# Optimization experiments

Hardware: AMD Instinct MI355X
Metric: run time of the kernel (lower is better)

## Reference

```python
import jax, jax.numpy as jnp
import numpy as np

N_NODES = 50000
N_EDGES = 800000
NFEAT = 128
NHID = 128
NCLASS = 2


def _glorot(key, shape):
    fan_in, fan_out = shape[0], shape[1]
    lim = np.sqrt(6.0 / (fan_in + fan_out)).astype(np.float32)
    return jax.random.uniform(key, shape, jnp.float32, -lim, lim)


def setup_inputs() -> dict:
    key = jax.random.key(0)
    ks = jax.random.split(key, 12)
    x = jax.random.normal(ks[0], (N_NODES, NFEAT), jnp.float32)
    edge_src = jax.random.randint(ks[1], (N_EDGES,), 0, N_NODES, jnp.int64)
    edge_dst = jax.random.randint(ks[2], (N_EDGES,), 0, N_NODES, jnp.int64)
    return {
        "x": x,
        "edge_src": edge_src,
        "edge_dst": edge_dst,
        "W1_self": _glorot(ks[3], (NFEAT, NHID)),
        "W1_neigh": _glorot(ks[4], (NFEAT, NHID)),
        "b1": jnp.zeros((NHID,), jnp.float32),
        "W2_self": _glorot(ks[5], (NHID, NHID)),
        "W2_neigh": _glorot(ks[6], (NHID, NHID)),
        "b2": jnp.zeros((NHID,), jnp.float32),
        "Wf": _glorot(ks[7], (NHID, NCLASS)),
        "bf": jnp.zeros((NCLASS,), jnp.float32),
    }


def _mean_neigh(h, edge_src, edge_dst):
    # gather source features per edge, segment-mean into destination nodes
    msgs = h[edge_src]                                   # [E, d]
    summed = jax.ops.segment_sum(msgs, edge_dst, num_segments=N_NODES)  # [N, d]
    deg = jax.ops.segment_sum(jnp.ones((edge_dst.shape[0],), h.dtype), edge_dst,
                              num_segments=N_NODES)      # [N]
    return summed / jnp.maximum(deg, 1.0)[:, None]


def _sage_conv(h, edge_src, edge_dst, W_self, W_neigh, b):
    h_neigh = _mean_neigh(h, edge_src, edge_dst)
    return h @ W_self + h_neigh @ W_neigh + b


def reference(x, edge_src, edge_dst, W1_self, W1_neigh, b1,
              W2_self, W2_neigh, b2, Wf, bf):
    h = jax.nn.relu(_sage_conv(x, edge_src, edge_dst, W1_self, W1_neigh, b1))
    # dropout is identity in eval mode
    h = _sage_conv(h, edge_src, edge_dst, W2_self, W2_neigh, b2)
    return h @ Wf + bf
```

## Files before the change

kernel.cpp:

```cpp
#include <hip/hip_runtime.h>
#include <cstdint>
#include <cstddef>

#define N_NODES 50000
#define N_EDGES 800000
#define CAP 64

#define BIN_SZ 512
#define NBIN 98
#define NSLOT 64

#define CHUNK_A 2048
#define N_PARTS 391

#define NB_PART N_PARTS
#define NB_PACK 128
#define NB_COMB 2
#define NB_PRE  (NB_PART + NB_PACK + NB_COMB)

#define NB_GEMM 391
#define NB_MAIN (NBIN * 5)

#define NB_AGG 13312

typedef __attribute__((ext_vector_type(8))) short bf16x8;
typedef __attribute__((ext_vector_type(4))) float f32x4;
typedef __attribute__((ext_vector_type(2))) float f32x2;
typedef __attribute__((ext_vector_type(4))) int   i32x4;

__device__ __forceinline__ unsigned short f2bf(float f) {
    unsigned u = __builtin_bit_cast(unsigned, f);
    u += 0x7fff + ((u >> 16) & 1);
    return (unsigned short)(u >> 16);
}
__device__ __forceinline__ float bflo(unsigned u) { return __builtin_bit_cast(float, u << 16); }
__device__ __forceinline__ float bfhi(unsigned u) { return __builtin_bit_cast(float, u & 0xffff0000u); }

__device__ __forceinline__ unsigned char f2fp8_sw(float f) {
    unsigned u = __builtin_bit_cast(unsigned, f);
    unsigned s = (u >> 24) & 0x80;
    unsigned a = u & 0x7fffffffu;
    if (a < 0x3c800000u) return (unsigned char)s;
    if (a > 0x43e00000u) a = 0x43e00000u;
    unsigned lsb = (a >> 20) & 1;
    a += 0x7ffffu + lsb;
    unsigned e = (a >> 23) - 120;
    unsigned m = (a >> 20) & 7;
    return (unsigned char)(s | (e << 3) | m);
}
__device__ __forceinline__ float fp82f_sw(unsigned b) {
    unsigned s = (b & 0x80u) << 24;
    unsigned e = (b >> 3) & 15, m = b & 7;
    if (e == 0) {
        float v = (float)m * 0.001953125f;
        return (b & 0x80u) ? -v : v;
    }
    return __builtin_bit_cast(float, s | ((e + 120) << 23) | (m << 20));
}
__device__ __forceinline__ unsigned short pk_fp8(float a, float b) {
#if __has_builtin(__builtin_amdgcn_cvt_pk_fp8_f32)
    return (unsigned short)__builtin_amdgcn_cvt_pk_fp8_f32(a, b, 0u, false);
#else
    return (unsigned short)(f2fp8_sw(a) | ((unsigned)f2fp8_sw(b) << 8));
#endif
}
__device__ __forceinline__ f32x2 unpk_fp8(unsigned short v) {
#if __has_builtin(__builtin_amdgcn_cvt_pk_f32_fp8)
    return __builtin_amdgcn_cvt_pk_f32_fp8((unsigned)v, false);
#else
    f32x2 r; r[0] = fp82f_sw(v & 0xffu); r[1] = fp82f_sw(v >> 8); return r;
#endif
}

__global__ __launch_bounds__(256) void k_pre(const int* __restrict__ src,
                                             const int* __restrict__ dst,
                                             const float* __restrict__ W1s,
                                             const float* __restrict__ W1n,
                                             const float* __restrict__ W2s,
                                             const float* __restrict__ W2n,
                                             const float* __restrict__ b2,
                                             const float* __restrict__ Wf,
                                             const float* __restrict__ bf,
                                             unsigned* __restrict__ seg,
                                             int* __restrict__ segcnt,
                                             unsigned short* __restrict__ wpack,
                                             float* __restrict__ wc) {
    int blk = blockIdx.x;
    int tid = threadIdx.x;

    if (blk < NB_PART) {
        __shared__ int hist[NBIN];
        for (int i = tid; i < NBIN; i += 256) hist[i] = 0;
        __syncthreads();
        int g = blk;
        int e0 = g * CHUNK_A + tid * 8;
        bool v = e0 < N_EDGES;
        i32x4 da = {0,0,0,0}, db = da, sa = da, sb = da;
        if (v) {
            da = *(const i32x4*)(dst + e0);
            db = *(const i32x4*)(dst + e0 + 4);
            sa = *(const i32x4*)(src + e0);
            sb = *(const i32x4*)(src + e0 + 4);
        }
        int d[8], s[8];
#pragma unroll
        for (int j = 0; j < 4; ++j) { d[j] = da[j]; s[j] = sa[j]; d[4 + j] = db[j]; s[4 + j] = sb[j]; }
#pragma unroll
        for (int j = 0; j < 8; ++j) {
            if (v) {
                int b = (int)((unsigned)d[j] >> 9);
                int lpos = atomicAdd(&hist[b], 1);
                if (lpos < NSLOT)
                    seg[((size_t)b * N_PARTS + g) * NSLOT + lpos] =
                        ((unsigned)d[j] << 16) | (unsigned)s[j];
            }
        }
        __syncthreads();
        for (int i = tid; i < NBIN; i += 256) {
            int h = hist[i];
            segcnt[i * N_PARTS + g] = h < NSLOT ? h : NSLOT;
        }
    } else if (blk < NB_PART + NB_PACK) {
        int idx = (blk - NB_PART) * 256 + tid;
        int j = idx & 7;
        int lane = (idx >> 3) & 63;
        int ks = (idx >> 9) & 7;
        int nt = idx >> 12;
        int krow = ks * 32 + ((lane >> 4) << 3) + j;
        int col = nt * 16 + (lane & 15);
        float v = (krow < 128) ? W1s[krow * 128 + col] : W1n[(krow - 128) * 128 + col];
        wpack[idx] = f2bf(v);
    } else {
        int role = blk - NB_PART - NB_PACK;
        int k = tid >> 1, c = tid & 1;
        const float* W = role == 0 ? W2s : W2n;
        float s = 0.f;
        for (int j = 0; j < 128; ++j) s += W[k * 128 + j] * Wf[j * 2 + c];
        wc[role * 256 + k * 2 + c] = s;
        if (role == 1 && tid < 2) {
            float sb = bf[tid];
            for (int j = 0; j < 128; ++j) sb += b2[j] * Wf[j * 2 + tid];
            wc[512 + tid] = sb;
        }
    }
}

__global__ __launch_bounds__(512) void k_main(const float* __restrict__ x,
                                              const unsigned* __restrict__ seg,
                                              const int* __restrict__ segcnt,
                                              const unsigned short* __restrict__ wpack,
                                              const float* __restrict__ b1,
                                              int* __restrict__ cnt,
                                              unsigned short* __restrict__ bucket,
                                              unsigned short* __restrict__ zb,
                                              unsigned char* __restrict__ yb8) {
    int blk = blockIdx.x;
    int tid = threadIdx.x;
    int G = blk / 5;
    int pos = blk - G * 5;

    if (pos == 0) {
        int b = G;
        __shared__ int cur[BIN_SZ];
        __shared__ int scnt[N_PARTS];
        for (int i = tid; i < BIN_SZ; i += 512) cur[i] = 0;
        for (int i = tid; i < N_PARTS; i += 512) scnt[i] = segcnt[b * N_PARTS + i];
        __syncthreads();
        int wave = tid >> 6, lane = tid & 63;
        const unsigned* segb = seg + (size_t)b * N_PARTS * NSLOT;
        for (int j = 0; j < 13; ++j) {
            unsigned v[4];
#pragma unroll
            for (int t = 0; t < 4; ++t) {
                int p = wave + 8 * (j * 4 + t);
                int n = p < N_PARTS ? scnt[p] : 0;
                v[t] = lane < n ? segb[(size_t)p * NSLOT + lane] : 0xffffffffu;
            }
#pragma unroll
            for (int t = 0; t < 4; ++t) {
                if (v[t] != 0xffffffffu) {
                    int d = (int)(v[t] >> 16);
                    int p = atomicAdd(&cur[d & (BIN_SZ - 1)], 1);
                    if (p < CAP) bucket[(size_t)d * CAP + p] = (unsigned short)(v[t] & 0xffffu);
                }
            }
        }
        __syncthreads();
        for (int i = tid; i < BIN_SZ; i += 512) {
            int node = (b << 9) + i;
            if (node < N_NODES) cnt[node] = cur[i];
        }
    } else {
        int g4 = G * 4 + (pos - 1);
        if (g4 >= NB_GEMM) return;
        int wid = tid >> 6;
        int lane = tid & 63;
        int l15 = lane & 15;
        int rowBase = g4 * 128 + wid * 16;
        int arow = rowBase + l15;
        if (arow >= N_NODES) arow = N_NODES - 1;
        int koff = (lane >> 4) << 3;

        const float* xrow = x + (size_t)arow * 128 + koff;
        bf16x8 a[4];
#pragma unroll
        for (int ks = 0; ks < 4; ++ks) {
            f32x4 f0 = *(const f32x4*)(xrow + ks * 32);
            f32x4 f1 = *(const f32x4*)(xrow + ks * 32 + 4);
            bf16x8 t;
            t[0] = (short)f2bf(f0[0]); t[1] = (short)f2bf(f0[1]);
            t[2] = (short)f2bf(f0[2]); t[3] = (short)f2bf(f0[3]);
            t[4] = (short)f2bf(f1[0]); t[5] = (short)f2bf(f1[1]);
            t[6] = (short)f2bf(f1[2]); t[7] = (short)f2bf(f1[3]);
            a[ks] = t;
        }

        f32x4 zacc[8] = {};
        f32x4 yacc[8] = {};
        const bf16x8* wp = (const bf16x8*)wpack + lane;
        __builtin_amdgcn_s_setprio(1);
#pragma unroll
        for (int nt = 0; nt < 8; ++nt) {
#pragma unroll
            for (int ks = 0; ks < 4; ++ks)
                zacc[nt] = __builtin_amdgcn_mfma_f32_16x16x32_bf16(a[ks], wp[(nt * 8 + ks) * 64], zacc[nt], 0, 0, 0);
#pragma unroll
            for (int ks = 0; ks < 4; ++ks)
                yacc[nt] = __builtin_amdgcn_mfma_f32_16x16x32_bf16(a[ks], wp[(nt * 8 + 4 + ks) * 64], yacc[nt], 0, 0, 0);
        }
        __builtin_amdgcn_s_setprio(0);

        int crow0 = rowBase + ((lane >> 4) << 2);
#pragma unroll
        for (int k = 0; k < 4; ++k) {
            int colA = k * 32 + l15;
            float biasA = b1[colA];
            float biasB = b1[colA + 16];
            int p2 = k * 16 + l15;
#pragma unroll
            for (int r = 0; r < 4; ++r) {
                int row = crow0 + r;
                if (row < N_NODES) {
                    unsigned zu = (unsigned)f2bf(zacc[2 * k][r] + biasA) |
                                  ((unsigned)f2bf(zacc[2 * k + 1][r] + biasB) << 16);
                    *(unsigned*)(zb + (size_t)row * 128 + 2 * p2) = zu;
                    *(unsigned short*)(yb8 + (size_t)row * 128 + 2 * p2) =
                        pk_fp8(yacc[2 * k][r], yacc[2 * k + 1][r]);
                }
            }
        }
    }
}

__global__ __launch_bounds__(256) void k_agg2(const unsigned char* __restrict__ yb8,
                                              const unsigned short* __restrict__ zb,
                                              const int* __restrict__ cnt,
                                              const unsigned short* __restrict__ bucket,
                                              const float* __restrict__ wc,
                                              float* __restrict__ pq) {
    int blk = blockIdx.x;
    int wavein = threadIdx.x >> 6;
    int lane = threadIdx.x & 63;
    int xcd = blk & 7;
    int i = (blk >> 3) * 4 + wavein;
    int b = xcd + ((i >> 9) << 3);
    if (b >= NBIN) return;
    int node = (b << 9) + (i & 511);
    if (node >= N_NODES) return;

    int deg = cnt[node];
    int colA = ((lane >> 4) << 5) + (lane & 15);
    int colB = colA + 16;
    unsigned zu = *(const unsigned*)(zb + (size_t)node * 128 + 2 * lane);
    float2 wsA = *(const float2*)(wc + 2 * colA);
    float2 wsB = *(const float2*)(wc + 2 * colB);
    float2 wnA = *(const float2*)(wc + 256 + 2 * colA);
    float2 wnB = *(const float2*)(wc + 256 + 2 * colB);

    int n = deg < CAP ? deg : CAP;
    const unsigned short* bk = bucket + (size_t)node * CAP;
    const unsigned char* ybl = yb8 + 2 * lane;
    float ax0 = 0.f, ay0 = 0.f, ax1 = 0.f, ay1 = 0.f;
    float ax2 = 0.f, ay2 = 0.f, ax3 = 0.f, ay3 = 0.f;
    int e = 0;
    for (; e + 16 <= n; e += 16) {
        uint4 ia = *(const uint4*)(bk + e);
        uint4 ib = *(const uint4*)(bk + e + 8);
        int s0  = ia.x & 0xffff, s1  = ia.x >> 16, s2  = ia.y & 0xffff, s3  = ia.y >> 16;
        int s4  = ia.z & 0xffff, s5  = ia.z >> 16, s6  = ia.w & 0xffff, s7  = ia.w >> 16;
        int s8  = ib.x & 0xffff, s9  = ib.x >> 16, s10 = ib.y & 0xffff, s11 = ib.y >> 16;
        int s12 = ib.z & 0xffff, s13 = ib.z >> 16, s14 = ib.w & 0xffff, s15 = ib.w >> 16;
        unsigned short t0  = *(const unsigned short*)(ybl + (size_t)s0  * 128);
        unsigned short t1  = *(const unsigned short*)(ybl + (size_t)s1  * 128);
        unsigned short t2  = *(const unsigned short*)(ybl + (size_t)s2  * 128);
        unsigned short t3  = *(const unsigned short*)(ybl + (size_t)s3  * 128);
        unsigned short t4  = *(const unsigned short*)(ybl + (size_t)s4  * 128);
        unsigned short t5  = *(const unsigned short*)(ybl + (size_t)s5  * 128);
        unsigned short t6  = *(const unsigned short*)(ybl + (size_t)s6  * 128);
        unsigned short t7  = *(const unsigned short*)(ybl + (size_t)s7  * 128);
        unsigned short t8  = *(const unsigned short*)(ybl + (size_t)s8  * 128);
        unsigned short t9  = *(const unsigned short*)(ybl + (size_t)s9  * 128);
        unsigned short t10 = *(const unsigned short*)(ybl + (size_t)s10 * 128);
        unsigned short t11 = *(const unsigned short*)(ybl + (size_t)s11 * 128);
        unsigned short t12 = *(const unsigned short*)(ybl + (size_t)s12 * 128);
        unsigned short t13 = *(const unsigned short*)(ybl + (size_t)s13 * 128);
        unsigned short t14 = *(const unsigned short*)(ybl + (size_t)s14 * 128);
        unsigned short t15 = *(const unsigned short*)(ybl + (size_t)s15 * 128);
        f32x2 v0 = unpk_fp8(t0),  v1 = unpk_fp8(t1),  v2 = unpk_fp8(t2),  v3 = unpk_fp8(t3);
        f32x2 v4 = unpk_fp8(t4),  v5 = unpk_fp8(t5),  v6 = unpk_fp8(t6),  v7 = unpk_fp8(t7);
        f32x2 v8 = unpk_fp8(t8),  v9 = unpk_fp8(t9),  v10 = unpk_fp8(t10), v11 = unpk_fp8(t11);
        f32x2 v12 = unpk_fp8(t12), v13 = unpk_fp8(t13), v14 = unpk_fp8(t14), v15 = unpk_fp8(t15);
        ax0 += v0[0];  ay0 += v0[1];  ax1 += v1[0];  ay1 += v1[1];
        ax2 += v2[0];  ay2 += v2[1];  ax3 += v3[0];  ay3 += v3[1];
        ax0 += v4[0];  ay0 += v4[1];  ax1 += v5[0];  ay1 += v5[1];
        ax2 += v6[0];  ay2 += v6[1];  ax3 += v7[0];  ay3 += v7[1];
        ax0 += v8[0];  ay0 += v8[1];  ax1 += v9[0];  ay1 += v9[1];
        ax2 += v10[0]; ay2 += v10[1]; ax3 += v11[0]; ay3 += v11[1];
        ax0 += v12[0]; ay0 += v12[1]; ax1 += v13[0]; ay1 += v13[1];
        ax2 += v14[0]; ay2 += v14[1]; ax3 += v15[0]; ay3 += v15[1];
    }
    if (e + 8 <= n) {
        uint4 ia = *(const uint4*)(bk + e);
        int s0 = ia.x & 0xffff, s1 = ia.x >> 16, s2 = ia.y & 0xffff, s3 = ia.y >> 16;
        int s4 = ia.z & 0xffff, s5 = ia.z >> 16, s6 = ia.w & 0xffff, s7 = ia.w >> 16;
        unsigned short t0 = *(const unsigned short*)(ybl + (size_t)s0 * 128);
        unsigned short t1 = *(const unsigned short*)(ybl + (size_t)s1 * 128);
        unsigned short t2 = *(const unsigned short*)(ybl + (size_t)s2 * 128);
        unsigned short t3 = *(const unsigned short*)(ybl + (size_t)s3 * 128);
        unsigned short t4 = *(const unsigned short*)(ybl + (size_t)s4 * 128);
        unsigned short t5 = *(const unsigned short*)(ybl + (size_t)s5 * 128);
        unsigned short t6 = *(const unsigned short*)(ybl + (size_t)s6 * 128);
        unsigned short t7 = *(const unsigned short*)(ybl + (size_t)s7 * 128);
        f32x2 v0 = unpk_fp8(t0), v1 = unpk_fp8(t1), v2 = unpk_fp8(t2), v3 = unpk_fp8(t3);
        f32x2 v4 = unpk_fp8(t4), v5 = unpk_fp8(t5), v6 = unpk_fp8(t6), v7 = unpk_fp8(t7);
        ax0 += v0[0]; ay0 += v0[1]; ax1 += v1[0]; ay1 += v1[1];
        ax2 += v2[0]; ay2 += v2[1]; ax3 += v3[0]; ay3 += v3[1];
        ax0 += v4[0]; ay0 += v4[1]; ax1 += v5[0]; ay1 += v5[1];
        ax2 += v6[0]; ay2 += v6[1]; ax3 += v7[0]; ay3 += v7[1];
        e += 8;
    }
    if (e + 4 <= n) {
        uint2 ia = *(const uint2*)(bk + e);
        int s0 = ia.x & 0xffff, s1 = ia.x >> 16, s2 = ia.y & 0xffff, s3 = ia.y >> 16;
        unsigned short t0 = *(const unsigned short*)(ybl + (size_t)s0 * 128);
        unsigned short t1 = *(const unsigned short*)(ybl + (size_t)s1 * 128);
        unsigned short t2 = *(const unsigned short*)(ybl + (size_t)s2 * 128);
        unsigned short t3 = *(const unsigned short*)(ybl + (size_t)s3 * 128);
        f32x2 v0 = unpk_fp8(t0), v1 = unpk_fp8(t1), v2 = unpk_fp8(t2), v3 = unpk_fp8(t3);
        ax0 += v0[0]; ay0 += v0[1]; ax1 += v1[0]; ay1 += v1[1];
        ax2 += v2[0]; ay2 += v2[1]; ax3 += v3[0]; ay3 += v3[1];
        e += 4;
    }
    for (; e < n; ++e) {
        unsigned short t = *(const unsigned short*)(ybl + (size_t)bk[e] * 128);
        f32x2 v = unpk_fp8(t);
        ax0 += v[0]; ay0 += v[1];
    }
    float inv = 1.0f / fmaxf((float)deg, 1.0f);
    float mx = ((ax0 + ax1) + (ax2 + ax3)) * inv;
    float my = ((ay0 + ay1) + (ay2 + ay3)) * inv;

    float h0 = fmaxf(bflo(zu) + mx, 0.f);
    float h1v = fmaxf(bfhi(zu) + my, 0.f);

    float p0 = h0 * wsA.x + h1v * wsB.x;
    float p1 = h0 * wsA.y + h1v * wsB.y;
    float q0 = h0 * wnA.x + h1v * wnB.x;
    float q1 = h0 * wnA.y + h1v * wnB.y;
#pragma unroll
    for (int off = 32; off >= 1; off >>= 1) {
        p0 += __shfl_xor(p0, off, 64);
        p1 += __shfl_xor(p1, off, 64);
        q0 += __shfl_xor(q0, off, 64);
        q1 += __shfl_xor(q1, off, 64);
    }
    if (lane == 0) {
        float4 o; o.x = p0; o.y = p1; o.z = q0; o.w = q1;
        ((float4*)pq)[node] = o;
    }
}

__global__ __launch_bounds__(256) void k_final(const float* __restrict__ pq,
                                               const int* __restrict__ cnt,
                                               const unsigned short* __restrict__ bucket,
                                               const float* __restrict__ wc,
                                               float* __restrict__ out) {
    int blk = blockIdx.x;
    int wavein = threadIdx.x >> 6;
    int lane = threadIdx.x & 63;
    int xcd = blk & 7;
    int i = (blk >> 3) * 4 + wavein;
    int b = xcd + ((i >> 9) << 3);
    if (b >= NBIN) return;
    int node = (b << 9) + (i & 511);
    if (node >= N_NODES) return;

    int deg = cnt[node];
    int n = deg < CAP ? deg : CAP;
    float qx = 0.f, qy = 0.f;
    if (lane < n) {
        int s = bucket[(size_t)node * CAP + lane];
        float2 q = *(const float2*)(pq + (size_t)s * 4 + 2);
        qx = q.x; qy = q.y;
    }
#pragma unroll
    for (int off = 32; off >= 1; off >>= 1) {
        qx += __shfl_xor(qx, off, 64);
        qy += __shfl_xor(qy, off, 64);
    }
    if (lane == 0) {
        float inv = 1.0f / fmaxf((float)deg, 1.0f);
        float2 p = *(const float2*)(pq + (size_t)node * 4);
        out[(size_t)node * 2 + 0] = p.x + qx * inv + wc[512];
        out[(size_t)node * 2 + 1] = p.y + qy * inv + wc[513];
    }
}

extern "C" void kernel_launch(void* const* d_in, const int* in_sizes, int n_in,
                              void* d_out, int out_size, void* d_ws, size_t ws_size,
                              hipStream_t stream) {
    const float* x   = (const float*)d_in[0];
    const int* esrc  = (const int*)d_in[1];
    const int* edst  = (const int*)d_in[2];
    const float* W1s = (const float*)d_in[3];
    const float* W1n = (const float*)d_in[4];
    const float* b1  = (const float*)d_in[5];
    const float* W2s = (const float*)d_in[6];
    const float* W2n = (const float*)d_in[7];
    const float* b2  = (const float*)d_in[8];
    const float* Wf  = (const float*)d_in[9];
    const float* bf  = (const float*)d_in[10];
    float* out = (float*)d_out;

    char* ws = (char*)d_ws;
    auto alloc = [&](size_t bytes) {
        char* p = ws;
        ws += (bytes + 255) & ~(size_t)255;
        return p;
    };
    int*            cnt    = (int*)           alloc((size_t)N_NODES * 4);
    unsigned short* bucket = (unsigned short*)alloc((size_t)N_NODES * CAP * 2);
    unsigned*       seg    = (unsigned*)      alloc((size_t)NBIN * N_PARTS * NSLOT * 4);
    int*            segcnt = (int*)           alloc((size_t)NBIN * N_PARTS * 4);
    unsigned short* zb     = (unsigned short*)alloc((size_t)N_NODES * 128 * 2);
    unsigned char*  yb8    = (unsigned char*) alloc((size_t)N_NODES * 128);
    unsigned short* wpack  = (unsigned short*)alloc(8 * 8 * 64 * 8 * 2);
    float*          pq     = (float*)         alloc((size_t)N_NODES * 4 * 4);
    float*          wc     = (float*)         alloc(1024 * 4);

    k_pre<<<NB_PRE, 256, 0, stream>>>(esrc, edst, W1s, W1n, W2s, W2n, b2, Wf, bf,
                                      seg, segcnt, wpack, wc);
    k_main<<<NB_MAIN, 512, 0, stream>>>(x, seg, segcnt, wpack, b1, cnt, bucket, zb, yb8);
    k_agg2<<<NB_AGG, 256, 0, stream>>>(yb8, zb, cnt, bucket, wc, pq);
    k_final<<<NB_AGG, 256, 0, stream>>>(pq, cnt, bucket, wc, out);
}
```

Before: 77.56 us.

## Fuse edge partitioning with layer-1 GEMM and pack weights into LDS per block

Restructures the kernel schedule so the edge partitioning and the dense layer-1 GEMM run in one front kernel, interleaved across blocks. Each GEMM block now packs W1 into bf16 in LDS itself, which removes the global wpack buffer and its dependency between kernels. The bucket build moves into its own small kernel. In exchange, every GEMM block redundantly converts 64KB of weights and the front kernel reserves 64KB of shared memory, which can reduce occupancy.

```diff
diff --git a/kernel.cpp b/kernel.cpp
--- a/kernel.cpp
+++ b/kernel.cpp
@@ -13,13 +13,10 @@
 #define CHUNK_A 2048
 #define N_PARTS 391
 
-#define NB_PART N_PARTS
-#define NB_PACK 128
-#define NB_COMB 2
-#define NB_PRE  (NB_PART + NB_PACK + NB_COMB)
-
 #define NB_GEMM 391
-#define NB_MAIN (NBIN * 5)
+#define NB_FRONT (2 * N_PARTS + 2)
+
+#define NB_BUILD NBIN
 
 #define NB_AGG 13312
 
@@ -72,131 +69,72 @@
 #endif
 }
 
-__global__ __launch_bounds__(256) void k_pre(const int* __restrict__ src,
-                                             const int* __restrict__ dst,
-                                             const float* __restrict__ W1s,
-                                             const float* __restrict__ W1n,
-                                             const float* __restrict__ W2s,
-                                             const float* __restrict__ W2n,
-                                             const float* __restrict__ b2,
-                                             const float* __restrict__ Wf,
-                                             const float* __restrict__ bf,
-                                             unsigned* __restrict__ seg,
-                                             int* __restrict__ segcnt,
-                                             unsigned short* __restrict__ wpack,
-                                             float* __restrict__ wc) {
+__global__ __launch_bounds__(512) void k_front(const float* __restrict__ x,
+                                               const int* __restrict__ src,
+                                               const int* __restrict__ dst,
+                                               const float* __restrict__ W1s,
+                                               const float* __restrict__ W1n,
+                                               const float* __restrict__ b1,
+                                               const float* __restrict__ W2s,
+                                               const float* __restrict__ W2n,
+                                               const float* __restrict__ b2,
+                                               const float* __restrict__ Wf,
+                                               const float* __restrict__ bf,
+                                               unsigned* __restrict__ seg,
+                                               int* __restrict__ segcnt,
+                                               unsigned short* __restrict__ zb,
+                                               unsigned char* __restrict__ yb8,
+                                               float* __restrict__ wc) {
+    __shared__ short wlds[32768];
     int blk = blockIdx.x;
     int tid = threadIdx.x;
 
-    if (blk < NB_PART) {
-        __shared__ int hist[NBIN];
-        for (int i = tid; i < NBIN; i += 256) hist[i] = 0;
+    if (blk < 2 * N_PARTS && (blk & 1) == 0) {
+        int g = blk >> 1;
+        int* hist = (int*)wlds;
+        for (int i = tid; i < NBIN; i += 512) hist[i] = 0;
         __syncthreads();
-        int g = blk;
-        int e0 = g * CHUNK_A + tid * 8;
+        int e0 = g * CHUNK_A + tid * 4;
         bool v = e0 < N_EDGES;
-        i32x4 da = {0,0,0,0}, db = da, sa = da, sb = da;
+        i32x4 d4 = {0,0,0,0}, s4 = d4;
         if (v) {
-            da = *(const i32x4*)(dst + e0);
-            db = *(const i32x4*)(dst + e0 + 4);
-            sa = *(const i32x4*)(src + e0);
-            sb = *(const i32x4*)(src + e0 + 4);
-        }
-        int d[8], s[8];
-#pragma unroll
-        for (int j = 0; j < 4; ++j) { d[j] = da[j]; s[j] = sa[j]; d[4 + j] = db[j]; s[4 + j] = sb[j]; }
-#pragma unroll
-        for (int j = 0; j < 8; ++j) {
+            d4 = *(const i32x4*)(dst + e0);
+            s4 = *(const i32x4*)(src + e0);
+        }
+#pragma unroll
+        for (int j = 0; j < 4; ++j) {
             if (v) {
-                int b = (int)((unsigned)d[j] >> 9);
+                int b = (int)((unsigned)d4[j] >> 9);
                 int lpos = atomicAdd(&hist[b], 1);
                 if (lpos < NSLOT)
                     seg[((size_t)b * N_PARTS + g) * NSLOT + lpos] =
-                        ((unsigned)d[j] << 16) | (unsigned)s[j];
+                        ((unsigned)d4[j] << 16) | (unsigned)s4[j];
             }
         }
         __syncthreads();
-        for (int i = tid; i < NBIN; i += 256) {
+        for (int i = tid; i < NBIN; i += 512) {
             int h = hist[i];
             segcnt[i * N_PARTS + g] = h < NSLOT ? h : NSLOT;
         }
-    } else if (blk < NB_PART + NB_PACK) {
-        int idx = (blk - NB_PART) * 256 + tid;
-        int j = idx & 7;
-        int lane = (idx >> 3) & 63;
-        int ks = (idx >> 9) & 7;
-        int nt = idx >> 12;
-        int krow = ks * 32 + ((lane >> 4) << 3) + j;
-        int col = nt * 16 + (lane & 15);
-        float v = (krow < 128) ? W1s[krow * 128 + col] : W1n[(krow - 128) * 128 + col];
-        wpack[idx] = f2bf(v);
-    } else {
-        int role = blk - NB_PART - NB_PACK;
-        int k = tid >> 1, c = tid & 1;
-        const float* W = role == 0 ? W2s : W2n;
-        float s = 0.f;
-        for (int j = 0; j < 128; ++j) s += W[k * 128 + j] * Wf[j * 2 + c];
-        wc[role * 256 + k * 2 + c] = s;
-        if (role == 1 && tid < 2) {
-            float sb = bf[tid];
-            for (int j = 0; j < 128; ++j) sb += b2[j] * Wf[j * 2 + tid];
-            wc[512 + tid] = sb;
-        }
-    }
-}
-
-__global__ __launch_bounds__(512) void k_main(const float* __restrict__ x,
-                                              const unsigned* __restrict__ seg,
-                                              const int* __restrict__ segcnt,
-                                              const unsigned short* __restrict__ wpack,
-                                              const float* __restrict__ b1,
-                                              int* __restrict__ cnt,
-                                              unsigned short* __restrict__ bucket,
-                                              unsigned short* __restrict__ zb,
-                                              unsigned char* __restrict__ yb8) {
-    int blk = blockIdx.x;
-    int tid = threadIdx.x;
-    int G = blk / 5;
-    int pos = blk - G * 5;
-
-    if (pos == 0) {
-        int b = G;
-        __shared__ int cur[BIN_SZ];
-        __shared__ int scnt[N_PARTS];
-        for (int i = tid; i < BIN_SZ; i += 512) cur[i] = 0;
-        for (int i = tid; i < N_PARTS; i += 512) scnt[i] = segcnt[b * N_PARTS + i];
+    } else if (blk < 2 * N_PARTS) {
+        int g4 = blk >> 1;
+        for (int i = 0; i < 64; ++i) {
+            int idx = i * 512 + tid;
+            int j = idx & 7;
+            int ln = (idx >> 3) & 63;
+            int ks = (idx >> 9) & 7;
+            int nt = idx >> 12;
+            int krow = ks * 32 + ((ln >> 4) << 3) + j;
+            int col = nt * 16 + (ln & 15);
+            float v = (krow < 128) ? W1s[krow * 128 + col] : W1n[(krow - 128) * 128 + col];
+            wlds[idx] = (short)f2bf(v);
+        }
         __syncthreads();
-        int wave = tid >> 6, lane = tid & 63;
-        const unsigned* segb = seg + (size_t)b * N_PARTS * NSLOT;
-        for (int j = 0; j < 13; ++j) {
-            unsigned v[4];
-#pragma unroll
-            for (int t = 0; t < 4; ++t) {
-                int p = wave + 8 * (j * 4 + t);
-                int n = p < N_PARTS ? scnt[p] : 0;
-                v[t] = lane < n ? segb[(size_t)p * NSLOT + lane] : 0xffffffffu;
-            }
-#pragma unroll
-            for (int t = 0; t < 4; ++t) {
-                if (v[t] != 0xffffffffu) {
-                    int d = (int)(v[t] >> 16);
-                    int p = atomicAdd(&cur[d & (BIN_SZ - 1)], 1);
-                    if (p < CAP) bucket[(size_t)d * CAP + p] = (unsigned short)(v[t] & 0xffffu);
-                }
-            }
-        }
-        __syncthreads();
-        for (int i = tid; i < BIN_SZ; i += 512) {
-            int node = (b << 9) + i;
-            if (node < N_NODES) cnt[node] = cur[i];
-        }
-    } else {
-        int g4 = G * 4 + (pos - 1);
-        if (g4 >= NB_GEMM) return;
-        int wid = tid >> 6;
+
+        int wavein = tid >> 6;
         int lane = tid & 63;
         int l15 = lane & 15;
-        int rowBase = g4 * 128 + wid * 16;
+        int rowBase = g4 * 128 + wavein * 16;
         int arow = rowBase + l15;
         if (arow >= N_NODES) arow = N_NODES - 1;
         int koff = (lane >> 4) << 3;
@@ -217,7 +155,7 @@
 
         f32x4 zacc[8] = {};
         f32x4 yacc[8] = {};
-        const bf16x8* wp = (const bf16x8*)wpack + lane;
+        const bf16x8* wp = (const bf16x8*)wlds + lane;
         __builtin_amdgcn_s_setprio(1);
 #pragma unroll
         for (int nt = 0; nt < 8; ++nt) {
@@ -249,6 +187,57 @@
                 }
             }
         }
+    } else {
+        int role = blk - 2 * N_PARTS;
+        if (tid < 256) {
+            int k = tid >> 1, c = tid & 1;
+            const float* W = role == 0 ? W2s : W2n;
+            float s = 0.f;
+            for (int j = 0; j < 128; ++j) s += W[k * 128 + j] * Wf[j * 2 + c];
+            wc[role * 256 + k * 2 + c] = s;
+            if (role == 1 && tid < 2) {
+                float sb = bf[tid];
+                for (int j = 0; j < 128; ++j) sb += b2[j] * Wf[j * 2 + tid];
+                wc[512 + tid] = sb;
+            }
+        }
+    }
+}
+
+__global__ __launch_bounds__(512) void k_build(const unsigned* __restrict__ seg,
+                                               const int* __restrict__ segcnt,
+                                               int* __restrict__ cnt,
+                                               unsigned short* __restrict__ bucket) {
+    int b = blockIdx.x;
+    int tid = threadIdx.x;
+    __shared__ int cur[BIN_SZ];
+    __shared__ int scnt[N_PARTS];
+    for (int i = tid; i < BIN_SZ; i += 512) cur[i] = 0;
+    for (int i = tid; i < N_PARTS; i += 512) scnt[i] = segcnt[b * N_PARTS + i];
+    __syncthreads();
+    int wave = tid >> 6, lane = tid & 63;
+    const unsigned* segb = seg + (size_t)b * N_PARTS * NSLOT;
+    for (int j = 0; j < 13; ++j) {
+        unsigned v[4];
+#pragma unroll
+        for (int t = 0; t < 4; ++t) {
+            int p = wave + 8 * (j * 4 + t);
+            int n = p < N_PARTS ? scnt[p] : 0;
+            v[t] = lane < n ? segb[(size_t)p * NSLOT + lane] : 0xffffffffu;
+        }
+#pragma unroll
+        for (int t = 0; t < 4; ++t) {
+            if (v[t] != 0xffffffffu) {
+                int d = (int)(v[t] >> 16);
+                int p = atomicAdd(&cur[d & (BIN_SZ - 1)], 1);
+                if (p < CAP) bucket[(size_t)d * CAP + p] = (unsigned short)(v[t] & 0xffffu);
+            }
+        }
+    }
+    __syncthreads();
+    for (int i = tid; i < BIN_SZ; i += 512) {
+        int node = (b << 9) + i;
+        if (node < N_NODES) cnt[node] = cur[i];
     }
 }
 
@@ -444,13 +433,12 @@
     int*            segcnt = (int*)           alloc((size_t)NBIN * N_PARTS * 4);
     unsigned short* zb     = (unsigned short*)alloc((size_t)N_NODES * 128 * 2);
     unsigned char*  yb8    = (unsigned char*) alloc((size_t)N_NODES * 128);
-    unsigned short* wpack  = (unsigned short*)alloc(8 * 8 * 64 * 8 * 2);
     float*          pq     = (float*)         alloc((size_t)N_NODES * 4 * 4);
     float*          wc     = (float*)         alloc(1024 * 4);
 
-    k_pre<<<NB_PRE, 256, 0, stream>>>(esrc, edst, W1s, W1n, W2s, W2n, b2, Wf, bf,
-                                      seg, segcnt, wpack, wc);
-    k_main<<<NB_MAIN, 512, 0, stream>>>(x, seg, segcnt, wpack, b1, cnt, bucket, zb, yb8);
+    k_front<<<NB_FRONT, 512, 0, stream>>>(x, esrc, edst, W1s, W1n, b1, W2s, W2n, b2, Wf, bf,
+                                          seg, segcnt, zb, yb8, wc);
+    k_build<<<NB_BUILD, 512, 0, stream>>>(seg, segcnt, cnt, bucket);
     k_agg2<<<NB_AGG, 256, 0, stream>>>(yb8, zb, cnt, bucket, wc, pq);
     k_final<<<NB_AGG, 256, 0, stream>>>(pq, cnt, bucket, wc, out);
 }
```

Result: slower. 104.6 us (+34.9%).
